# Optimization experiments

Hardware: AMD Instinct MI355X
Metric: run time of the kernel (lower is better)

## Reference

```python
import jax, jax.numpy as jnp
import numpy as np

D, H, N, K = 1024, 2048, 8, 2
B, S = 4, 2048

def setup_inputs() -> dict:
    key = jax.random.key(0)
    ks = jax.random.split(key, 4)
    x = jax.random.normal(ks[0], (B, S, D), dtype=jnp.float32)
    Wr = jax.random.normal(ks[1], (N, D), dtype=jnp.float32) / np.sqrt(D)
    br = jnp.zeros((N,), jnp.float32)
    Wl1 = jax.random.normal(ks[2], (N, D, 2 * H), dtype=jnp.float32) / np.sqrt(D)
    bl1 = jnp.zeros((N, 2 * H), jnp.float32)
    Wl2 = jax.random.normal(ks[3], (N, H, D), dtype=jnp.float32) / np.sqrt(H)
    bl2 = jnp.zeros((N, D), jnp.float32)
    biases_N = jnp.zeros((N,), jnp.float32)
    return {"x": x, "Wr": Wr, "br": br, "Wl1": Wl1, "bl1": bl1,
            "Wl2": Wl2, "bl2": bl2, "biases_N": biases_N}

def reference(x, Wr, br, Wl1, bl1, Wl2, bl2, biases_N):
    Bb, Ss, Dd = x.shape
    # router: Linear(D, N)
    scores_BSN = jnp.einsum('bsd,nd->bsn', x, Wr) + br
    w_BSN = jax.nn.softmax(scores_BSN, axis=-1)
    _, idx_BSK = jax.lax.top_k(scores_BSN + biases_N[None, None, :], K)
    val_BSK = jnp.take_along_axis(w_BSN, idx_BSK, axis=-1)
    val_BSK = val_BSK / jnp.sum(val_BSK, axis=-1, keepdims=True)

    M = Bb * Ss
    x_MD = x.reshape(M, Dd)
    idx_MK = idx_BSK.reshape(M, K)
    val_MK = val_BSK.reshape(M, K)

    # dense all-expert SwiGLU: h_NM2H -> silu(a)*b -> y_NMD
    h_NM2H = jnp.einsum('md,ndh->nmh', x_MD, Wl1) + bl1[:, None, :]
    a_NMH, b_NMH = h_NM2H[..., :H], h_NM2H[..., H:]
    y_NMD = jnp.einsum('nmh,nhd->nmd', jax.nn.silu(a_NMH) * b_NMH, Wl2) + bl2[:, None, :]

    # scatter top-k weights into dense [M, N] then weighted combine
    ew_MN = jnp.zeros((M, N), x.dtype)
    ew_MN = ew_MN.at[jnp.arange(M)[:, None], idx_MK].set(val_MK)
    y_MD = jnp.einsum('mn,nmd->md', ew_MN, y_NMD)
    return y_MD.reshape(Bb, Ss, Dd)
```

## Files before the change

### kernel.cpp

```cpp
#include <hip/hip_runtime.h>
#include <hip/hip_bf16.h>

#define D_ 1024
#define H_ 2048
#define H2_ 4096
#define NE 8
#define M_ 8192
#define RBMAX 72

typedef short v8s __attribute__((ext_vector_type(8)));
typedef float v4f __attribute__((ext_vector_type(4)));

typedef const __attribute__((address_space(1))) void gvoid_t;
typedef __attribute__((address_space(3))) void svoid_t;

__device__ __forceinline__ unsigned short f2b(float f) {
    __hip_bfloat16 h = __float2bfloat16(f);
    unsigned short u;
    __builtin_memcpy(&u, &h, sizeof(u));
    return u;
}

__global__ __launch_bounds__(256) void router_score_kernel(
    const float* __restrict__ x, const float* __restrict__ Wr,
    const float* __restrict__ br, const float* __restrict__ biases,
    int* __restrict__ pick, float* __restrict__ slot_w,
    unsigned short* __restrict__ xb) {
    int wid = threadIdx.x >> 6;
    int lane = threadIdx.x & 63;
    int m = blockIdx.x * 4 + wid;
    if (m >= M_) return;
    const float4* xr = (const float4*)(x + (size_t)m * D_);
    float4 xv[4];
#pragma unroll
    for (int p = 0; p < 4; ++p) xv[p] = xr[p * 64 + lane];
    ushort4* xbr = (ushort4*)(xb + (size_t)m * D_);
#pragma unroll
    for (int p = 0; p < 4; ++p) {
        ushort4 o;
        o.x = f2b(xv[p].x); o.y = f2b(xv[p].y); o.z = f2b(xv[p].z); o.w = f2b(xv[p].w);
        xbr[p * 64 + lane] = o;
    }
    float s[NE];
#pragma unroll
    for (int n = 0; n < NE; ++n) {
        const float4* wr = (const float4*)(Wr + (size_t)n * D_);
        float acc = 0.f;
#pragma unroll
        for (int p = 0; p < 4; ++p) {
            float4 w4 = wr[p * 64 + lane];
            acc += xv[p].x * w4.x + xv[p].y * w4.y + xv[p].z * w4.z + xv[p].w * w4.w;
        }
#pragma unroll
        for (int off = 32; off; off >>= 1) acc += __shfl_xor(acc, off, 64);
        s[n] = acc + br[n];
    }
    if (lane == 0) {
        float t[NE];
#pragma unroll
        for (int n = 0; n < NE; ++n) t[n] = s[n] + biases[n];
        int i0 = 0;
#pragma unroll
        for (int n = 1; n < NE; ++n) if (t[n] > t[i0]) i0 = n;
        int i1 = -1;
#pragma unroll
        for (int n = 0; n < NE; ++n) {
            if (n == i0) continue;
            if (i1 < 0 || t[n] > t[i1]) i1 = n;
        }
        float mx = fmaxf(s[i0], s[i1]);
        float e0 = expf(s[i0] - mx), e1 = expf(s[i1] - mx);
        float inv = 1.f / (e0 + e1);
        pick[m] = i0 | (i1 << 4);
        slot_w[m * 2] = e0 * inv;
        slot_w[m * 2 + 1] = e1 * inv;
    }
}

__global__ __launch_bounds__(256) void hist_kernel(const int* __restrict__ pick,
                                                   int* __restrict__ blkcnt) {
    __shared__ int h[NE];
    int t = threadIdx.x;
    if (t < NE) h[t] = 0;
    __syncthreads();
    int idx = blockIdx.x * 256 + t;
    int e = (pick[idx >> 1] >> ((idx & 1) * 4)) & 15;
    atomicAdd(&h[e], 1);
    __syncthreads();
    if (t < NE) blkcnt[blockIdx.x * NE + t] = h[t];
}

__global__ void scan_kernel(const int* __restrict__ blkcnt, int* __restrict__ blkoff,
                            int* __restrict__ cnt, int* __restrict__ bp) {
    int e = threadIdx.x;
    if (e < NE) {
        int run = 0;
        for (int b = 0; b < 64; ++b) {
            blkoff[b * NE + e] = run;
            run += blkcnt[b * NE + e];
        }
        cnt[e] = run;
    }
    __syncthreads();
    if (e == 0) {
        int b = 0, r = 0;
        for (int n = 0; n < NE; ++n) {
            bp[n] = b; bp[16 + n] = r;
            b += ((cnt[n] + 255) / 256) * 256;
            r += cnt[n];
        }
        bp[NE] = b; bp[16 + NE] = r;
    }
}

__global__ __launch_bounds__(256) void scatter_kernel(
    const int* __restrict__ pick, const int* __restrict__ blkoff,
    int* __restrict__ perm, int* __restrict__ slot_idx) {
    __shared__ int wvcnt[4 * NE];
    int t = threadIdx.x, lane = t & 63, w = t >> 6;
    int idx = blockIdx.x * 256 + t;
    int m = idx >> 1, sl = idx & 1;
    int e = (pick[m] >> (sl * 4)) & 15;
    unsigned long long ltm = (1ull << lane) - 1;
    int my = 0;
#pragma unroll
    for (int ee = 0; ee < NE; ++ee) {
        unsigned long long mask = __ballot(e == ee);
        if (ee == e) my = __popcll(mask & ltm);
        if (lane == ee) wvcnt[w * NE + ee] = __popcll(mask);
    }
    __syncthreads();
    int off = blkoff[blockIdx.x * NE + e] + my;
    for (int w2 = 0; w2 < w; ++w2) off += wvcnt[w2 * NE + e];
    perm[e * M_ + off] = m;
    slot_idx[m * 2 + sl] = (e << 13) | off;
}

__global__ __launch_bounds__(256) void pack_w1_kernel(const float* __restrict__ Wl1,
                                                      unsigned short* __restrict__ W1P) {
    int jb = blockIdx.x, t = blockIdx.y, e = blockIdx.z;
    int tid = threadIdx.x;
    int lr = tid;
    int q = lr >> 7;
    int h = jb * 128 + (tid & 127);
    size_t srcb = ((size_t)e * D_ + t * 64) * H2_ + (size_t)q * H_ + h;
    unsigned short* dst = W1P + ((((size_t)(e * 16 + jb) * 16 + t) * 2 + q) << 13) + ((lr & 127) * 8) * 8;
    int sw = lr & 7;
    v8s v;
#pragma unroll 2
    for (int g = 0; g < 8; ++g) {
#pragma unroll
        for (int j = 0; j < 8; ++j) {
            float f = Wl1[srcb + (size_t)(g * 8 + j) * H2_];
            v[j] = (short)f2b(f);
        }
        *(v8s*)(dst + (size_t)(g ^ sw) * 8) = v;
    }
}

__global__ __launch_bounds__(256) void pack_w2_kernel(const float* __restrict__ Wl2,
                                                      unsigned short* __restrict__ W2P) {
    int jb = blockIdx.x, t = blockIdx.y, e = blockIdx.z;
    int tid = threadIdx.x;
    int row = tid & 127, half = tid >> 7;
    int col = jb * 128 + row;
    unsigned short* dst = W2P + ((size_t)(e * 8 + jb) * 32 + t) * 8192 + row * 64;
#pragma unroll
    for (int gg = 0; gg < 4; ++gg) {
        int g = half * 4 + gg;
        int kgrp = g ^ (row & 7);
        v8s v;
#pragma unroll
        for (int j = 0; j < 8; ++j) {
            float f = Wl2[((size_t)e * H_ + t * 64 + kgrp * 8 + j) * D_ + col];
            v[j] = (short)f2b(f);
        }
        *(v8s*)(dst + g * 8) = v;
    }
}

#define GLDS(src, dst) __builtin_amdgcn_global_load_lds((gvoid_t*)(src), (svoid_t*)(dst), 16, 0, 0)
#define STB_(dstbase, t, q) { const unsigned short* s_ = Bsrc + (((size_t)(t) * 2 + (q)) << 13) + tid * 8; \
    GLDS(s_, (dstbase) + (q) * 8192 + tid * 8); \
    GLDS(s_ + 4096, (dstbase) + (q) * 8192 + 4096 + tid * 8); }
#define STA_X(dstbase, t, q) { \
    GLDS(aptr[q][0] + (size_t)(t) * 64, (dstbase) + (q) * 8192 + tid * 8); \
    GLDS(aptr[q][1] + (size_t)(t) * 64, (dstbase) + (q) * 8192 + 4096 + tid * 8); }

#define PHASE(Ab, Bb, QM, QN, LA, LB, STAGE_STMT, VM4) do { \
    if (LA) { _Pragma("unroll") for (int i_ = 0; i_ < 4; ++i_) { \
        const unsigned short* ar_ = (Ab) + ((QM) * 128 + wm * 64 + i_ * 16 + fr) * 64; \
        a_[i_][0] = *(const v8s*)(ar_ + s0); a_[i_][1] = *(const v8s*)(ar_ + s1); } } \
    if (LB) { _Pragma("unroll") for (int n_ = 0; n_ < 2; ++n_) { \
        const unsigned short* br_ = (Bb) + ((QN) * 128 + wn * 32 + n_ * 16 + fr) * 64; \
        b_[n_][0] = *(const v8s*)(br_ + s0); b_[n_][1] = *(const v8s*)(br_ + s1); } } \
    STAGE_STMT; \
    __builtin_amdgcn_s_setprio(1); \
    _Pragma("unroll") for (int kk_ = 0; kk_ < 2; ++kk_) \
        _Pragma("unroll") for (int i_ = 0; i_ < 4; ++i_) \
            _Pragma("unroll") for (int n_ = 0; n_ < 2; ++n_) \
                acc[(QM) * 4 + i_][(QN) * 2 + n_] = __builtin_amdgcn_mfma_f32_16x16x32_bf16( \
                    a_[i_][kk_], b_[n_][kk_], acc[(QM) * 4 + i_][(QN) * 2 + n_], 0, 0, 0); \
    __builtin_amdgcn_s_setprio(0); \
    __builtin_amdgcn_sched_barrier(0); \
    if (VM4) { asm volatile("s_waitcnt vmcnt(4)" ::: "memory"); } \
    __builtin_amdgcn_s_barrier(); \
    __builtin_amdgcn_sched_barrier(0); \
} while (0)

__global__ __launch_bounds__(512, 2) void gemm1_kernel(
    const unsigned short* __restrict__ xb, const unsigned short* __restrict__ Bpack,
    const float* __restrict__ bias, const int* __restrict__ cnt, const int* __restrict__ bp,
    const int* __restrict__ perm, unsigned short* __restrict__ actP) {
    constexpr int NT = 16;
    int p = blockIdx.x;
    int tm = (p >> 3) & 31;
    int pid = (p & 7) + ((p >> 8) << 3);
    int e = pid >> 4;
    int jb = pid & 15;
    int cn = cnt[e];
    if (tm * 256 >= cn) return;
    int rb = (bp[e] >> 8) + tm;

    __shared__ __align__(16) unsigned short SH[66560];
    unsigned short* As0 = SH;
    unsigned short* As1 = SH + 16384;
    unsigned short* Bs0 = SH + 32768;
    unsigned short* Bs1 = SH + 49152;

    int tid = threadIdx.x, lane = tid & 63, wid = tid >> 6;
    int wm = wid >> 2, wn = wid & 3;
    int fr = lane & 15, fg = lane >> 4;
    int swz = fr & 7;
    int s0 = (fg ^ swz) * 8;
    int s1 = ((4 + fg) ^ swz) * 8;

    int kgs = tid & 7;
    const unsigned short* aptr[2][2];
#pragma unroll
    for (int q = 0; q < 2; ++q)
#pragma unroll
        for (int h = 0; h < 2; ++h) {
            int lr = q * 128 + h * 64 + (tid >> 3);
            int r = ((lr >> 6) & 1) * 128 + ((lr >> 7) & 1) * 64 + (lr & 63);
            int rl = min(tm * 256 + r, cn - 1);
            int tok = perm[e * M_ + rl];
            aptr[q][h] = xb + (size_t)tok * D_ + ((kgs ^ (lr & 7)) << 3);
        }

    const unsigned short* Bsrc = Bpack + (((size_t)(e * 16 + jb) * NT) << 14);

    v4f acc[8][4] = {};
    v8s a_[4][2];
    v8s b_[2][2];

    STA_X(As0, 0, 0); STB_(Bs0, 0, 1); STA_X(As0, 0, 1); STB_(Bs0, 0, 0);
    STA_X(As1, 1, 0); STB_(Bs1, 1, 1);
    asm volatile("s_waitcnt vmcnt(0)" ::: "memory");
    __builtin_amdgcn_s_barrier();
    __builtin_amdgcn_sched_barrier(0);

    for (int i2 = 0; i2 < NT / 2; ++i2) {
        int T1 = 2 * i2 + 1;
        int T2c = min(2 * i2 + 2, NT - 1);
        int T3c = min(2 * i2 + 3, NT - 1);
        PHASE(As0, Bs0, 0, 0, 1, 1, STB_(Bs1, T1, 0), 0);
        PHASE(As0, Bs0, 0, 1, 0, 1, STA_X(As1, T1, 1), 0);
        PHASE(As0, Bs0, 1, 1, 1, 0, STA_X(As0, T2c, 0), 0);
        PHASE(As0, Bs0, 1, 0, 0, 1, STB_(Bs0, T2c, 1), 1);
        PHASE(As1, Bs1, 0, 0, 1, 1, STB_(Bs0, T2c, 0), 0);
        PHASE(As1, Bs1, 0, 1, 0, 1, STA_X(As0, T2c, 1), 0);
        PHASE(As1, Bs1, 1, 1, 1, 0, STA_X(As1, T3c, 0), 0);
        PHASE(As1, Bs1, 1, 0, 0, 1, STB_(Bs1, T3c, 1), 1);
    }
    asm volatile("s_waitcnt vmcnt(0)" ::: "memory");
    __syncthreads();

    unsigned short* actl = SH;
    int hl0 = wn * 32 + fr, hl1 = wn * 32 + 16 + fr;
    float ba0 = bias[e * H2_ + jb * 128 + hl0];
    float bb0 = bias[e * H2_ + H_ + jb * 128 + hl0];
    float ba1 = bias[e * H2_ + jb * 128 + hl1];
    float bb1 = bias[e * H2_ + H_ + jb * 128 + hl1];
#pragma unroll
    for (int I = 0; I < 8; ++I) {
        int r0 = wm * 128 + (I >> 2) * 64 + (I & 3) * 16 + fg * 4;
#pragma unroll
        for (int rr = 0; rr < 4; ++rr) {
            float a0 = acc[I][0][rr] + ba0, b0 = acc[I][2][rr] + bb0;
            float a1 = acc[I][1][rr] + ba1, b1 = acc[I][3][rr] + bb1;
            actl[(r0 + rr) * 136 + hl0] = f2b(a0 / (1.f + __expf(-a0)) * b0);
            actl[(r0 + rr) * 136 + hl1] = f2b(a1 / (1.f + __expf(-a1)) * b1);
        }
    }
    __syncthreads();
#pragma unroll
    for (int c8 = 0; c8 < 8; ++c8) {
        int cid = c8 * 512 + tid;
        int t2l = cid >> 11, rem = cid & 2047;
        int q = rem >> 10, s = rem & 1023;
        int lr = q * 128 + (s >> 3);
        int g = (s & 7) ^ (lr & 7);
        int r = ((lr >> 6) & 1) * 128 + (lr >> 7) * 64 + (lr & 63);
        v8s v = *(const v8s*)(actl + r * 136 + t2l * 64 + g * 8);
        *(v8s*)(actP + ((((size_t)rb * 32 + jb * 2 + t2l) * 2 + q) << 13) + s * 8) = v;
    }
}

#define STAH2(dst, t, q) { const unsigned short* s_ = Asrc + (((size_t)(t) * 2 + (q)) << 13) + tid * 8; \
    GLDS(s_, (dst) + (q) * 8192 + tid * 8); \
    GLDS(s_ + 4096, (dst) + (q) * 8192 + 4096 + tid * 8); }
#define STBH2(dst, t, h) { const unsigned short* s_ = Bsrc + ((size_t)(t) * 8192) + (h) * 4096 + tid * 8; \
    GLDS(s_, (dst) + (h) * 4096 + tid * 8); }

#define PHASE2(Ab, Bp_, QM, LB, STAGE_STMT) do { \
    _Pragma("unroll") for (int i_ = 0; i_ < 4; ++i_) { \
        const unsigned short* ar_ = (Ab) + ((QM) * 128 + wm * 64 + i_ * 16 + fr) * 64; \
        a_[i_][0] = *(const v8s*)(ar_ + s0); a_[i_][1] = *(const v8s*)(ar_ + s1); } \
    if (LB) { _Pragma("unroll") for (int n_ = 0; n_ < 2; ++n_) { \
        const unsigned short* br_ = (Bp_) + (wn * 32 + n_ * 16 + fr) * 64; \
        b_[n_][0] = *(const v8s*)(br_ + s0); b_[n_][1] = *(const v8s*)(br_ + s1); } } \
    STAGE_STMT; \
    __builtin_amdgcn_s_setprio(1); \
    _Pragma("unroll") for (int kk_ = 0; kk_ < 2; ++kk_) \
        _Pragma("unroll") for (int i_ = 0; i_ < 4; ++i_) \
            _Pragma("unroll") for (int n_ = 0; n_ < 2; ++n_) \
                acc[(QM) * 4 + i_][n_] = __builtin_amdgcn_mfma_f32_16x16x32_bf16( \
                    a_[i_][kk_], b_[n_][kk_], acc[(QM) * 4 + i_][n_], 0, 0, 0); \
    __builtin_amdgcn_s_setprio(0); \
    __builtin_amdgcn_sched_barrier(0); \
    asm volatile("s_waitcnt vmcnt(6)" ::: "memory"); \
    __builtin_amdgcn_s_barrier(); \
    __builtin_amdgcn_sched_barrier(0); \
} while (0)

__global__ __launch_bounds__(512, 2) void gemm2_kernel(
    const unsigned short* __restrict__ actP, const unsigned short* __restrict__ W2P,
    const float* __restrict__ bl2, const int* __restrict__ cnt, const int* __restrict__ bp,
    float* __restrict__ y) {
    constexpr int NT = 32;
    int p = blockIdx.x;
    int tm = (p >> 3) & 31;
    int pid = (p & 7) + ((p >> 8) << 3);
    int e = pid >> 3;
    int jb = pid & 7;
    int cn = cnt[e];
    if (tm * 256 >= cn) return;
    int rb = (bp[e] >> 8) + tm;

    __shared__ __align__(16) unsigned short SH[57344];
    unsigned short* As0 = SH;
    unsigned short* As1 = SH + 16384;
    unsigned short* Bb0 = SH + 32768;
    unsigned short* Bb1 = SH + 40960;
    unsigned short* Bb2 = SH + 49152;

    int tid = threadIdx.x, lane = tid & 63, wid = tid >> 6;
    int wm = wid >> 2, wn = wid & 3;
    int fr = lane & 15, fg = lane >> 4;
    int swz = fr & 7;
    int s0 = (fg ^ swz) * 8;
    int s1 = ((4 + fg) ^ swz) * 8;

    const unsigned short* Asrc = actP + ((size_t)rb << 19);
    const unsigned short* Bsrc = W2P + ((size_t)(e * 8 + jb) * 32) * 8192;

    v4f acc[8][2] = {};
    v8s a_[4][2];
    v8s b_[2][2];

    STAH2(As0, 0, 0); STAH2(As0, 0, 1);
    STBH2(Bb0, 0, 0); STBH2(Bb0, 0, 1);
    STAH2(As1, 1, 0);
    STBH2(Bb1, 1, 0); STBH2(Bb1, 1, 1);
    asm volatile("s_waitcnt vmcnt(0)" ::: "memory");
    __builtin_amdgcn_s_barrier();
    __builtin_amdgcn_sched_barrier(0);

    unsigned short* Bc0 = Bb0;
    unsigned short* Bc1 = Bb1;
    unsigned short* Bn = Bb2;
    for (int i2 = 0; i2 < NT / 2; ++i2) {
        int T1 = 2 * i2 + 1;
        int T2 = min(2 * i2 + 2, NT - 1);
        int T3 = min(2 * i2 + 3, NT - 1);
        PHASE2(As0, Bc0, 0, 1, { STAH2(As1, T1, 1); STBH2(Bn, T2, 0); });
        PHASE2(As0, Bc0, 1, 0, { STAH2(As0, T2, 0); STBH2(Bn, T2, 1); });
        PHASE2(As1, Bc1, 0, 1, { STAH2(As0, T2, 1); STBH2(Bc0, T3, 0); });
        PHASE2(As1, Bc1, 1, 0, { STAH2(As1, T3, 0); STBH2(Bc0, T3, 1); });
        unsigned short* oB0 = Bc0;
        Bc0 = Bn; Bn = Bc1; Bc1 = oB0;
    }
    asm volatile("s_waitcnt vmcnt(0)" ::: "memory");
    __syncthreads();

    float* yl = (float*)SH;
    int bsr = bp[16 + e];
    float b2_0 = bl2[e * D_ + jb * 128 + wn * 32 + fr];
    float b2_1 = bl2[e * D_ + jb * 128 + wn * 32 + 16 + fr];
#pragma unroll
    for (int wmp = 0; wmp < 2; ++wmp) {
        if (wm == wmp) {
#pragma unroll
            for (int I = 0; I < 8; ++I) {
                int r0 = (I >> 2) * 64 + (I & 3) * 16 + fg * 4;
#pragma unroll
                for (int rr = 0; rr < 4; ++rr) {
                    yl[(r0 + rr) * 132 + wn * 32 + fr] = acc[I][0][rr] + b2_0;
                    yl[(r0 + rr) * 132 + wn * 32 + 16 + fr] = acc[I][1][rr] + b2_1;
                }
            }
        }
        __syncthreads();
#pragma unroll
        for (int f = 0; f < 8; ++f) {
            int fid = f * 512 + tid;
            int row = fid >> 5, c4 = fid & 31;
            int rp = tm * 256 + wmp * 128 + row;
            if (rp < cn) {
                float4 v = *(const float4*)(yl + row * 132 + c4 * 4);
                *(float4*)(y + (size_t)(bsr + rp) * D_ + jb * 128 + c4 * 4) = v;
            }
        }
        __syncthreads();
    }
}

__global__ __launch_bounds__(256) void combine_kernel(
    const float* __restrict__ y, const int* __restrict__ slot_idx,
    const float* __restrict__ slot_w, const int* __restrict__ bp,
    float* __restrict__ out) {
    int m = blockIdx.x * 4 + (threadIdx.x >> 6);
    int t2 = threadIdx.x & 63;
    int i0 = slot_idx[m * 2], i1 = slot_idx[m * 2 + 1];
    float w0 = slot_w[m * 2], w1 = slot_w[m * 2 + 1];
    const float4* y0 = (const float4*)(y + (size_t)(bp[16 + (i0 >> 13)] + (i0 & (M_ - 1))) * D_);
    const float4* y1 = (const float4*)(y + (size_t)(bp[16 + (i1 >> 13)] + (i1 & (M_ - 1))) * D_);
    float4* o = (float4*)(out + (size_t)m * D_);
#pragma unroll
    for (int k = 0; k < 4; ++k) {
        int idx = k * 64 + t2;
        float4 a = y0[idx], b = y1[idx];
        float4 r;
        r.x = w0 * a.x + w1 * b.x;
        r.y = w0 * a.y + w1 * b.y;
        r.z = w0 * a.z + w1 * b.z;
        r.w = w0 * a.w + w1 * b.w;
        o[idx] = r;
    }
}

__global__ void ws_fail_kernel(float* __restrict__ out) {
    if (threadIdx.x == 0 && blockIdx.x == 0) out[0] = 1e30f;
}

extern "C" void kernel_launch(void* const* d_in, const int* in_sizes, int n_in,
                              void* d_out, int out_size, void* d_ws, size_t ws_size,
                              hipStream_t stream) {
    const float* x = (const float*)d_in[0];
    const float* Wr = (const float*)d_in[1];
    const float* br = (const float*)d_in[2];
    const float* Wl1 = (const float*)d_in[3];
    const float* bl1 = (const float*)d_in[4];
    const float* Wl2 = (const float*)d_in[5];
    const float* bl2 = (const float*)d_in[6];
    const float* biases = (const float*)d_in[7];
    float* out = (float*)d_out;

    char* ws = (char*)d_ws;
    size_t off = 0;
    auto alloc = [&](size_t bytes) {
        char* p = ws + off;
        off += (bytes + 255) & ~(size_t)255;
        return p;
    };
    unsigned short* W1P = (unsigned short*)alloc((size_t)NE * 16 * 16 * 2 * 8192 * 2);
    unsigned short* W2P = (unsigned short*)alloc((size_t)NE * 8 * 32 * 8192 * 2);
    unsigned short* xb = (unsigned short*)alloc((size_t)M_ * D_ * 2);
    unsigned short* actP = (unsigned short*)alloc((size_t)RBMAX * 32 * 2 * 8192 * 2);
    int* perm = (int*)alloc((size_t)NE * M_ * 4);
    int* slot_idx = (int*)alloc((size_t)M_ * 2 * 4);
    float* slot_w = (float*)alloc((size_t)M_ * 2 * 4);
    int* pick = (int*)alloc((size_t)M_ * 4);
    int* blkcnt = (int*)alloc(64 * NE * 4);
    int* blkoff = (int*)alloc(64 * NE * 4);
    int* cnt = (int*)alloc(256);
    int* bp = (int*)alloc(256);
    float* y = (float*)W1P;
    if (ws_size < off) {
        ws_fail_kernel<<<1, 64, 0, stream>>>(out);
        return;
    }

    pack_w1_kernel<<<dim3(16, 16, NE), 256, 0, stream>>>(Wl1, W1P);
    pack_w2_kernel<<<dim3(8, 32, NE), 256, 0, stream>>>(Wl2, W2P);
    router_score_kernel<<<M_ / 4, 256, 0, stream>>>(x, Wr, br, biases, pick, slot_w, xb);
    hist_kernel<<<64, 256, 0, stream>>>(pick, blkcnt);
    scan_kernel<<<1, 64, 0, stream>>>(blkcnt, blkoff, cnt, bp);
    scatter_kernel<<<64, 256, 0, stream>>>(pick, blkoff, perm, slot_idx);
    gemm1_kernel<<<32 * 16 * NE, 512, 0, stream>>>(xb, W1P, bl1, cnt, bp, perm, actP);
    gemm2_kernel<<<32 * 8 * NE, 512, 0, stream>>>(actP, W2P, bl2, cnt, bp, y);
    combine_kernel<<<M_ / 4, 256, 0, stream>>>(y, slot_idx, slot_w, bp, out);
}
```

Before: 407.2 us.

## Shrink gemm2 tile to 128x128 with 256 threads and simple double buffering

Restructures the down-projection GEMM from 256x128 tiles with 512 threads and a hand-scheduled triple-buffered B pipeline to 128x128 tiles with 256 threads and a plain double-buffered A/B loop. The grid doubles so more blocks cover the variable per-expert row counts, and LDS use drops, which may allow more resident blocks. The epilogue now writes accumulators straight to global memory instead of staging them through shared memory for float4 stores. In exchange, B weights are reloaded twice as often, each step waits on all loads (vmcnt(0)) which weakens overlap, and the global stores are narrower and less coalesced.

Result: slower. 415.7 us (+2.1%).

```diff
diff --git a/kernel.cpp b/kernel.cpp
--- a/kernel.cpp
+++ b/kernel.cpp
@@ -307,56 +307,29 @@
     }
 }
 
-#define STAH2(dst, t, q) { const unsigned short* s_ = Asrc + (((size_t)(t) * 2 + (q)) << 13) + tid * 8; \
-    GLDS(s_, (dst) + (q) * 8192 + tid * 8); \
-    GLDS(s_ + 4096, (dst) + (q) * 8192 + 4096 + tid * 8); }
-#define STBH2(dst, t, h) { const unsigned short* s_ = Bsrc + ((size_t)(t) * 8192) + (h) * 4096 + tid * 8; \
-    GLDS(s_, (dst) + (h) * 4096 + tid * 8); }
-
-#define PHASE2(Ab, Bp_, QM, LB, STAGE_STMT) do { \
-    _Pragma("unroll") for (int i_ = 0; i_ < 4; ++i_) { \
-        const unsigned short* ar_ = (Ab) + ((QM) * 128 + wm * 64 + i_ * 16 + fr) * 64; \
-        a_[i_][0] = *(const v8s*)(ar_ + s0); a_[i_][1] = *(const v8s*)(ar_ + s1); } \
-    if (LB) { _Pragma("unroll") for (int n_ = 0; n_ < 2; ++n_) { \
-        const unsigned short* br_ = (Bp_) + (wn * 32 + n_ * 16 + fr) * 64; \
-        b_[n_][0] = *(const v8s*)(br_ + s0); b_[n_][1] = *(const v8s*)(br_ + s1); } } \
-    STAGE_STMT; \
-    __builtin_amdgcn_s_setprio(1); \
-    _Pragma("unroll") for (int kk_ = 0; kk_ < 2; ++kk_) \
-        _Pragma("unroll") for (int i_ = 0; i_ < 4; ++i_) \
-            _Pragma("unroll") for (int n_ = 0; n_ < 2; ++n_) \
-                acc[(QM) * 4 + i_][n_] = __builtin_amdgcn_mfma_f32_16x16x32_bf16( \
-                    a_[i_][kk_], b_[n_][kk_], acc[(QM) * 4 + i_][n_], 0, 0, 0); \
-    __builtin_amdgcn_s_setprio(0); \
-    __builtin_amdgcn_sched_barrier(0); \
-    asm volatile("s_waitcnt vmcnt(6)" ::: "memory"); \
-    __builtin_amdgcn_s_barrier(); \
-    __builtin_amdgcn_sched_barrier(0); \
-} while (0)
-
-__global__ __launch_bounds__(512, 2) void gemm2_kernel(
+__global__ __launch_bounds__(256, 2) void gemm2_kernel(
     const unsigned short* __restrict__ actP, const unsigned short* __restrict__ W2P,
     const float* __restrict__ bl2, const int* __restrict__ cnt, const int* __restrict__ bp,
     float* __restrict__ y) {
     constexpr int NT = 32;
     int p = blockIdx.x;
-    int tm = (p >> 3) & 31;
-    int pid = (p & 7) + ((p >> 8) << 3);
+    int tm2 = (p >> 3) & 63;
+    int pid = (p & 7) + ((p >> 9) << 3);
     int e = pid >> 3;
     int jb = pid & 7;
     int cn = cnt[e];
-    if (tm * 256 >= cn) return;
-    int rb = (bp[e] >> 8) + tm;
-
-    __shared__ __align__(16) unsigned short SH[57344];
+    if (tm2 * 128 >= cn) return;
+    int rb = (bp[e] >> 8) + (tm2 >> 1);
+    int half = tm2 & 1;
+
+    __shared__ __align__(16) unsigned short SH[32768];
     unsigned short* As0 = SH;
-    unsigned short* As1 = SH + 16384;
-    unsigned short* Bb0 = SH + 32768;
-    unsigned short* Bb1 = SH + 40960;
-    unsigned short* Bb2 = SH + 49152;
+    unsigned short* As1 = SH + 8192;
+    unsigned short* Bs0 = SH + 16384;
+    unsigned short* Bs1 = SH + 24576;
 
     int tid = threadIdx.x, lane = tid & 63, wid = tid >> 6;
-    int wm = wid >> 2, wn = wid & 3;
+    int wm = wid >> 1, wn = wid & 1;
     int fr = lane & 15, fg = lane >> 4;
     int swz = fr & 7;
     int s0 = (fg ^ swz) * 8;
@@ -365,64 +338,67 @@
     const unsigned short* Asrc = actP + ((size_t)rb << 19);
     const unsigned short* Bsrc = W2P + ((size_t)(e * 8 + jb) * 32) * 8192;
 
-    v4f acc[8][2] = {};
-    v8s a_[4][2];
-    v8s b_[2][2];
-
-    STAH2(As0, 0, 0); STAH2(As0, 0, 1);
-    STBH2(Bb0, 0, 0); STBH2(Bb0, 0, 1);
-    STAH2(As1, 1, 0);
-    STBH2(Bb1, 1, 0); STBH2(Bb1, 1, 1);
+#define STG2(Ad, Bd, t) { \
+    _Pragma("unroll") for (int q_ = 0; q_ < 2; ++q_) \
+        _Pragma("unroll") for (int c_ = 0; c_ < 2; ++c_) { \
+            const unsigned short* sa_ = Asrc + (((size_t)(t) * 2 + q_) << 13) + half * 4096 + c_ * 2048 + tid * 8; \
+            GLDS(sa_, (Ad) + q_ * 4096 + c_ * 2048 + tid * 8); } \
+    _Pragma("unroll") for (int c_ = 0; c_ < 4; ++c_) { \
+        const unsigned short* sb_ = Bsrc + ((size_t)(t) * 8192) + c_ * 2048 + tid * 8; \
+        GLDS(sb_, (Bd) + c_ * 2048 + tid * 8); } }
+
+    v4f acc[4][4] = {};
+
+    STG2(As0, Bs0, 0);
     asm volatile("s_waitcnt vmcnt(0)" ::: "memory");
     __builtin_amdgcn_s_barrier();
     __builtin_amdgcn_sched_barrier(0);
 
-    unsigned short* Bc0 = Bb0;
-    unsigned short* Bc1 = Bb1;
-    unsigned short* Bn = Bb2;
-    for (int i2 = 0; i2 < NT / 2; ++i2) {
-        int T1 = 2 * i2 + 1;
-        int T2 = min(2 * i2 + 2, NT - 1);
-        int T3 = min(2 * i2 + 3, NT - 1);
-        PHASE2(As0, Bc0, 0, 1, { STAH2(As1, T1, 1); STBH2(Bn, T2, 0); });
-        PHASE2(As0, Bc0, 1, 0, { STAH2(As0, T2, 0); STBH2(Bn, T2, 1); });
-        PHASE2(As1, Bc1, 0, 1, { STAH2(As0, T2, 1); STBH2(Bc0, T3, 0); });
-        PHASE2(As1, Bc1, 1, 0, { STAH2(As1, T3, 0); STBH2(Bc0, T3, 1); });
-        unsigned short* oB0 = Bc0;
-        Bc0 = Bn; Bn = Bc1; Bc1 = oB0;
-    }
-    asm volatile("s_waitcnt vmcnt(0)" ::: "memory");
-    __syncthreads();
-
-    float* yl = (float*)SH;
+    int cur = 0;
+    for (int t = 0; t < NT; ++t) {
+        unsigned short* Ac = cur ? As1 : As0;
+        unsigned short* Bc = cur ? Bs1 : Bs0;
+        unsigned short* An = cur ? As0 : As1;
+        unsigned short* Bn = cur ? Bs0 : Bs1;
+        if (t + 1 < NT) STG2(An, Bn, t + 1);
+#pragma unroll
+        for (int kk = 0; kk < 2; ++kk) {
+            v8s a_[4], b_[4];
+            int ss = kk ? s1 : s0;
+#pragma unroll
+            for (int i = 0; i < 4; ++i)
+                a_[i] = *(const v8s*)(Ac + (wm * 64 + i * 16 + fr) * 64 + ss);
+#pragma unroll
+            for (int n = 0; n < 4; ++n)
+                b_[n] = *(const v8s*)(Bc + (wn * 64 + n * 16 + fr) * 64 + ss);
+            __builtin_amdgcn_s_setprio(1);
+#pragma unroll
+            for (int i = 0; i < 4; ++i)
+#pragma unroll
+                for (int n = 0; n < 4; ++n)
+                    acc[i][n] = __builtin_amdgcn_mfma_f32_16x16x32_bf16(a_[i], b_[n], acc[i][n], 0, 0, 0);
+            __builtin_amdgcn_s_setprio(0);
+        }
+        __builtin_amdgcn_sched_barrier(0);
+        asm volatile("s_waitcnt vmcnt(0)" ::: "memory");
+        __builtin_amdgcn_s_barrier();
+        __builtin_amdgcn_sched_barrier(0);
+        cur ^= 1;
+    }
+
     int bsr = bp[16 + e];
-    float b2_0 = bl2[e * D_ + jb * 128 + wn * 32 + fr];
-    float b2_1 = bl2[e * D_ + jb * 128 + wn * 32 + 16 + fr];
-#pragma unroll
-    for (int wmp = 0; wmp < 2; ++wmp) {
-        if (wm == wmp) {
-#pragma unroll
-            for (int I = 0; I < 8; ++I) {
-                int r0 = (I >> 2) * 64 + (I & 3) * 16 + fg * 4;
-#pragma unroll
-                for (int rr = 0; rr < 4; ++rr) {
-                    yl[(r0 + rr) * 132 + wn * 32 + fr] = acc[I][0][rr] + b2_0;
-                    yl[(r0 + rr) * 132 + wn * 32 + 16 + fr] = acc[I][1][rr] + b2_1;
-                }
+#pragma unroll
+    for (int n = 0; n < 4; ++n) {
+        int col = jb * 128 + wn * 64 + n * 16 + fr;
+        float b2 = bl2[e * D_ + col];
+#pragma unroll
+        for (int i = 0; i < 4; ++i)
+#pragma unroll
+            for (int rr = 0; rr < 4; ++rr) {
+                int rp = tm2 * 128 + wm * 64 + i * 16 + fg * 4 + rr;
+                if (rp < cn)
+                    y[(size_t)(bsr + rp) * D_ + col] = acc[i][n][rr] + b2;
             }
-        }
-        __syncthreads();
-#pragma unroll
-        for (int f = 0; f < 8; ++f) {
-            int fid = f * 512 + tid;
-            int row = fid >> 5, c4 = fid & 31;
-            int rp = tm * 256 + wmp * 128 + row;
-            if (rp < cn) {
-                float4 v = *(const float4*)(yl + row * 132 + c4 * 4);
-                *(float4*)(y + (size_t)(bsr + rp) * D_ + jb * 128 + c4 * 4) = v;
-            }
-        }
-        __syncthreads();
     }
 }
 
@@ -499,6 +475,6 @@
     scan_kernel<<<1, 64, 0, stream>>>(blkcnt, blkoff, cnt, bp);
     scatter_kernel<<<64, 256, 0, stream>>>(pick, blkoff, perm, slot_idx);
     gemm1_kernel<<<32 * 16 * NE, 512, 0, stream>>>(xb, W1P, bl1, cnt, bp, perm, actP);
-    gemm2_kernel<<<32 * 8 * NE, 512, 0, stream>>>(actP, W2P, bl2, cnt, bp, y);
+    gemm2_kernel<<<4096, 256, 0, stream>>>(actP, W2P, bl2, cnt, bp, y);
     combine_kernel<<<M_ / 4, 256, 0, stream>>>(y, slot_idx, slot_w, bp, out);
 }
```
